# Kernel tuning notes

Measured on AMD Instinct MI355X. Metric: run time of the kernel, lower is better.

The kernel has to match this reference:

```python
import jax, jax.numpy as jnp
import numpy as np

DELTA = 2.0

def _pearson(x, y):
    vx = x - jnp.mean(x)
    vy = y - jnp.mean(y)
    return jnp.sum(vx * vy) / (jnp.sqrt(jnp.sum(vx ** 2)) * jnp.sqrt(jnp.sum(vy ** 2)))

def setup_inputs() -> dict:
    key = jax.random.key(0)
    k1, k2 = jax.random.split(key)
    n = 4000000
    output = jax.random.normal(k1, (n, 6), dtype=jnp.float32)
    label = jax.random.normal(k2, (n, 1), dtype=jnp.float32)
    return {"output": output, "label": label}

def reference(output, label):
    # output: [n, 6] = [q0, q1, q2, q3, q4, q]; label: [n, 1]
    target = label[:, 0]  # [n]

    # Pearson correlation of each of the 6 prediction columns vs label
    plcc = [_pearson(output[:, i], target) for i in range(6)]

    # Per-sample weighted pseudo-Huber loss (vectorized over batch)
    diff = output - label                      # [n, 6] (pred - target)
    huber = DELTA ** 2 * (jnp.sqrt(1.0 + (diff / DELTA) ** 2) - 1.0)  # [n, 6]
    alpha_head = 0.2 * jnp.tanh(diff[:, :5]) ** 2                     # [n, 5]
    alpha = jnp.concatenate([alpha_head, jnp.ones_like(diff[:, 5:6])], axis=1)  # [n, 6]
    loss_old = jnp.mean(jnp.sum(huber * alpha, axis=1))

    p0, p1, p2, p3, p4, p5 = plcc
    s = 5.0 - p0 - p1 - p2 - p3 - p4
    plcc_pen = ((1 - p0) ** 2 + (1 - p1) ** 2 + (1 - p2) ** 2 + (1 - p3) ** 2 + (1 - p4) ** 2) / s
    loss = loss_old + plcc_pen + (1.0 - p5)
    return loss
```

## Files before the change

### kernel.cpp

```cpp
#include <hip/hip_runtime.h>
#include <math.h>

static constexpr int BLOCK     = 256;
static constexpr int NACC      = 21;
static constexpr int PSTRIDE   = 24;
static constexpr int TILE_ROWS = 1024;
static constexpr int TILE_F4   = TILE_ROWS * 6 / 4;
static constexpr int MAXBLOCKS = 2048;

__device__ __forceinline__ void async_f4(const float4* g, float4* l) {
    __builtin_amdgcn_global_load_lds(
        (const __attribute__((address_space(1))) void*)g,
        (__attribute__((address_space(3))) void*)l,
        16, 0, 0);
}

__device__ __forceinline__ float fast_tanh_sq(float d) {
    float e = __expf(2.0f * d);
    float r = __builtin_amdgcn_rcpf(e + 1.0f);
    float t = 1.0f - 2.0f * r;
    return t * t;
}

__device__ __forceinline__ void row_accum(float acc[NACC], const float x[6], float y) {
    acc[18] += y;
    acc[19] += y * y;
    float rowh = 0.0f;
#pragma unroll
    for (int c = 0; c < 6; ++c) {
        const float xv = x[c];
        acc[c]      += xv;
        acc[6 + c]  += xv * xv;
        acc[12 + c] += xv * y;
        const float d   = xv - y;
        const float hub = 4.0f * (__builtin_amdgcn_sqrtf(1.0f + 0.25f * d * d) - 1.0f);
        const float al  = (c < 5) ? (0.2f * fast_tanh_sq(d)) : 1.0f;
        rowh += hub * al;
    }
    acc[20] += rowh;
}

__device__ __forceinline__ void chunk_accum(float acc[NACC],
                                            const float4 a, const float4 b,
                                            const float4 c, const float2 y2) {
    const float r0v[6] = {a.x, a.y, a.z, a.w, b.x, b.y};
    const float r1v[6] = {b.z, b.w, c.x, c.y, c.z, c.w};
    row_accum(acc, r0v, y2.x);
    row_accum(acc, r1v, y2.y);
}

__global__ __launch_bounds__(BLOCK) void huber_partial_kernel(
    const float* __restrict__ out6,
    const float* __restrict__ lab,
    float* __restrict__ part,
    int n)
{
    __shared__ float4 tile[TILE_F4];
    __shared__ float  red[BLOCK / 64][NACC];

    float acc[NACC];
#pragma unroll
    for (int k = 0; k < NACC; ++k) acc[k] = 0.0f;

    const int t  = threadIdx.x;
    const int n2 = n & ~1;
    const int full_tiles = n2 / TILE_ROWS;
    const int tail_start = full_tiles * TILE_ROWS;

    const float4* gsrc = reinterpret_cast<const float4*>(out6);
    const float2* lab2 = reinterpret_cast<const float2*>(lab);

    for (int tl = blockIdx.x; tl < full_tiles; tl += gridDim.x) {
        const long long basef4 = (long long)tl * TILE_F4;

#pragma unroll
        for (int k = 0; k < 6; ++k)
            async_f4(&gsrc[basef4 + k * BLOCK + t], &tile[k * BLOCK + t]);

        const float2 yA = lab2[(size_t)tl * (TILE_ROWS / 2) + t];
        const float2 yB = lab2[(size_t)tl * (TILE_ROWS / 2) + BLOCK + t];

        __syncthreads();

        chunk_accum(acc, tile[3 * t + 0], tile[3 * t + 1], tile[3 * t + 2], yA);
        chunk_accum(acc, tile[TILE_F4 / 2 + 3 * t + 0],
                         tile[TILE_F4 / 2 + 3 * t + 1],
                         tile[TILE_F4 / 2 + 3 * t + 2], yB);

        __syncthreads();
    }

    if (blockIdx.x == 0) {
        for (int r = tail_start + 2 * t; r + 1 < n2 + 1; r += 2 * BLOCK) {
            if (r + 1 >= n2) break;
            const long long g = (long long)r * 3 / 2;
            chunk_accum(acc, gsrc[g], gsrc[g + 1], gsrc[g + 2], lab2[r >> 1]);
        }
        if ((n & 1) && t == 0) {
            const size_t row = (size_t)n - 1;
            float xr[6];
#pragma unroll
            for (int c = 0; c < 6; ++c) xr[c] = out6[row * 6 + c];
            row_accum(acc, xr, lab[row]);
        }
    }

#pragma unroll
    for (int k = 0; k < NACC; ++k) {
        float v = acc[k];
#pragma unroll
        for (int off = 32; off > 0; off >>= 1)
            v += __shfl_down(v, off, 64);
        acc[k] = v;
    }

    const int wave = t >> 6;
    const int lane = t & 63;
    if (lane == 0) {
#pragma unroll
        for (int k = 0; k < NACC; ++k) red[wave][k] = acc[k];
    }
    __syncthreads();
    if (t < NACC) {
        float s = 0.0f;
#pragma unroll
        for (int w = 0; w < BLOCK / 64; ++w) s += red[w][t];
        part[(size_t)blockIdx.x * PSTRIDE + t] = s;
    }
}

__global__ __launch_bounds__(BLOCK) void huber_final_kernel(
    const float* __restrict__ part, int nblocks, int n, float* __restrict__ out)
{
    __shared__ double sred[BLOCK / 64][NACC];

    double acc[NACC];
#pragma unroll
    for (int k = 0; k < NACC; ++k) acc[k] = 0.0;

    for (int b = threadIdx.x; b < nblocks; b += BLOCK) {
        const float* p = part + (size_t)b * PSTRIDE;
        const float4* p4 = reinterpret_cast<const float4*>(p);
#pragma unroll
        for (int q = 0; q < 5; ++q) {
            const float4 v = p4[q];
            acc[q * 4 + 0] += (double)v.x;
            acc[q * 4 + 1] += (double)v.y;
            acc[q * 4 + 2] += (double)v.z;
            acc[q * 4 + 3] += (double)v.w;
        }
        acc[20] += (double)p[20];
    }

#pragma unroll
    for (int k = 0; k < NACC; ++k) {
        double v = acc[k];
#pragma unroll
        for (int off = 32; off > 0; off >>= 1)
            v += __shfl_down(v, off, 64);
        acc[k] = v;
    }

    const int wave = threadIdx.x >> 6;
    const int lane = threadIdx.x & 63;
    if (lane == 0) {
#pragma unroll
        for (int k = 0; k < NACC; ++k) sred[wave][k] = acc[k];
    }
    __syncthreads();

    if (threadIdx.x == 0) {
        double tot[NACC];
#pragma unroll
        for (int k = 0; k < NACC; ++k) {
            double s = 0.0;
#pragma unroll
            for (int w = 0; w < BLOCK / 64; ++w) s += sred[w][k];
            tot[k] = s;
        }

        const double dn  = (double)n;
        const double Sy  = tot[18];
        const double Syy = tot[19];
        const double vary = Syy - Sy * Sy / dn;
        double pc[6];
#pragma unroll
        for (int c = 0; c < 6; ++c) {
            const double Sx  = tot[c];
            const double Sxx = tot[6 + c];
            const double Sxy = tot[12 + c];
            const double cov  = Sxy - Sx * Sy / dn;
            const double varx = Sxx - Sx * Sx / dn;
            pc[c] = cov / (sqrt(varx) * sqrt(vary));
        }
        const double loss_old = tot[20] / dn;
        const double s = 5.0 - pc[0] - pc[1] - pc[2] - pc[3] - pc[4];
        double pen = 0.0;
#pragma unroll
        for (int c = 0; c < 5; ++c) pen += (1.0 - pc[c]) * (1.0 - pc[c]);
        pen /= s;
        const double loss = loss_old + pen + (1.0 - pc[5]);
        out[0] = (float)loss;
    }
}

extern "C" void kernel_launch(void* const* d_in, const int* in_sizes, int n_in,
                              void* d_out, int out_size, void* d_ws, size_t ws_size,
                              hipStream_t stream) {
    const float* out6 = (const float*)d_in[0];
    const float* lab  = (const float*)d_in[1];
    float* out = (float*)d_out;
    const int n = in_sizes[1];

    const int n2 = n & ~1;
    int full_tiles = n2 / TILE_ROWS;
    if (full_tiles < 1) full_tiles = 1;

    int nblocks = MAXBLOCKS;
    const int maxb = (int)(ws_size / (PSTRIDE * sizeof(float)));
    if (nblocks > maxb)       nblocks = maxb;
    if (nblocks > full_tiles) nblocks = full_tiles;
    if (nblocks < 1)          nblocks = 1;

    float* part = (float*)d_ws;
    hipLaunchKernelGGL(huber_partial_kernel, dim3(nblocks), dim3(BLOCK), 0, stream,
                       out6, lab, part, n);
    hipLaunchKernelGGL(huber_final_kernel, dim3(1), dim3(BLOCK), 0, stream,
                       part, nblocks, n, out);
}
```

Baseline: 163.0 us.

## Double-buffer per-wave async LDS loads to overlap memory with compute

Replaces the block-wide tile loop, which used two __syncthreads per tile, with independent per-wave 128-row tiles that are double-buffered in LDS. The next tile's data and labels are fetched with async global_load_lds while the current tile is processed, and waves are ordered with s_waitcnt vmcnt instead of barriers. Labels now also go through LDS using 4-byte async loads. This aims to hide memory latency and remove block-level syncs, but it depends on the hand-written vmcnt counts being correct and makes the label loads much smaller.

```diff
diff --git a/kernel.cpp b/kernel.cpp
--- a/kernel.cpp
+++ b/kernel.cpp
@@ -1,18 +1,25 @@
 #include <hip/hip_runtime.h>
 #include <math.h>
 
-static constexpr int BLOCK     = 256;
-static constexpr int NACC      = 21;
-static constexpr int PSTRIDE   = 24;
-static constexpr int TILE_ROWS = 1024;
-static constexpr int TILE_F4   = TILE_ROWS * 6 / 4;
-static constexpr int MAXBLOCKS = 2048;
+static constexpr int BLOCK      = 256;
+static constexpr int WAVES      = BLOCK / 64;
+static constexpr int NACC       = 21;
+static constexpr int PSTRIDE    = 24;
+static constexpr int WTILE_ROWS = 128;
+static constexpr int WTILE_F4   = WTILE_ROWS * 6 / 4;
+static constexpr int MAXBLOCKS  = 2048;
 
 __device__ __forceinline__ void async_f4(const float4* g, float4* l) {
     __builtin_amdgcn_global_load_lds(
         (const __attribute__((address_space(1))) void*)g,
         (__attribute__((address_space(3))) void*)l,
         16, 0, 0);
+}
+__device__ __forceinline__ void async_f1(const float* g, float* l) {
+    __builtin_amdgcn_global_load_lds(
+        (const __attribute__((address_space(1))) void*)g,
+        (__attribute__((address_space(3))) void*)l,
+        4, 0, 0);
 }
 
 __device__ __forceinline__ float fast_tanh_sq(float d) {
@@ -55,53 +62,60 @@
     float* __restrict__ part,
     int n)
 {
-    __shared__ float4 tile[TILE_F4];
-    __shared__ float  red[BLOCK / 64][NACC];
+    __shared__ __align__(16) float4 sdat[WAVES][2][WTILE_F4];
+    __shared__ __align__(16) float  slab[WAVES][2][WTILE_ROWS];
+    __shared__ float red[WAVES][NACC];
 
     float acc[NACC];
 #pragma unroll
     for (int k = 0; k < NACC; ++k) acc[k] = 0.0f;
 
-    const int t  = threadIdx.x;
-    const int n2 = n & ~1;
-    const int full_tiles = n2 / TILE_ROWS;
-    const int tail_start = full_tiles * TILE_ROWS;
-
+    const int t = threadIdx.x;
+    const int w = t >> 6;
+    const int l = t & 63;
+
+    const long long tiles = (long long)n / WTILE_ROWS;
+    const int nws = gridDim.x * WAVES;
     const float4* gsrc = reinterpret_cast<const float4*>(out6);
-    const float2* lab2 = reinterpret_cast<const float2*>(lab);
-
-    for (int tl = blockIdx.x; tl < full_tiles; tl += gridDim.x) {
-        const long long basef4 = (long long)tl * TILE_F4;
-
-#pragma unroll
-        for (int k = 0; k < 6; ++k)
-            async_f4(&gsrc[basef4 + k * BLOCK + t], &tile[k * BLOCK + t]);
-
-        const float2 yA = lab2[(size_t)tl * (TILE_ROWS / 2) + t];
-        const float2 yB = lab2[(size_t)tl * (TILE_ROWS / 2) + BLOCK + t];
-
-        __syncthreads();
-
-        chunk_accum(acc, tile[3 * t + 0], tile[3 * t + 1], tile[3 * t + 2], yA);
-        chunk_accum(acc, tile[TILE_F4 / 2 + 3 * t + 0],
-                         tile[TILE_F4 / 2 + 3 * t + 1],
-                         tile[TILE_F4 / 2 + 3 * t + 2], yB);
-
-        __syncthreads();
-    }
-
-    if (blockIdx.x == 0) {
-        for (int r = tail_start + 2 * t; r + 1 < n2 + 1; r += 2 * BLOCK) {
-            if (r + 1 >= n2) break;
-            const long long g = (long long)r * 3 / 2;
-            chunk_accum(acc, gsrc[g], gsrc[g + 1], gsrc[g + 2], lab2[r >> 1]);
-        }
-        if ((n & 1) && t == 0) {
-            const size_t row = (size_t)n - 1;
+
+    auto issue = [&](long long tile, int b) {
+        const float4* g = gsrc + tile * WTILE_F4;
+        async_f4(g + l,       &sdat[w][b][l]);
+        async_f4(g + 64 + l,  &sdat[w][b][64 + l]);
+        async_f4(g + 128 + l, &sdat[w][b][128 + l]);
+        const float* gl = lab + tile * WTILE_ROWS;
+        async_f1(gl + l,      &slab[w][b][l]);
+        async_f1(gl + 64 + l, &slab[w][b][64 + l]);
+    };
+
+    long long tc = (long long)blockIdx.x * WAVES + w;
+    int buf = 0;
+    if (tc < tiles) issue(tc, buf);
+
+    while (tc < tiles) {
+        const long long tn = tc + nws;
+        if (tn < tiles) {
+            issue(tn, buf ^ 1);
+            asm volatile("s_waitcnt vmcnt(5)" ::: "memory");
+        } else {
+            asm volatile("s_waitcnt vmcnt(0)" ::: "memory");
+        }
+        const float4 a = sdat[w][buf][3 * l + 0];
+        const float4 b = sdat[w][buf][3 * l + 1];
+        const float4 c = sdat[w][buf][3 * l + 2];
+        const float2 y2 = make_float2(slab[w][buf][2 * l],
+                                      slab[w][buf][2 * l + 1]);
+        chunk_accum(acc, a, b, c, y2);
+        buf ^= 1;
+        tc = tn;
+    }
+
+    if (blockIdx.x == 0 && w == 0) {
+        for (long long r = tiles * WTILE_ROWS + l; r < n; r += 64) {
             float xr[6];
 #pragma unroll
-            for (int c = 0; c < 6; ++c) xr[c] = out6[row * 6 + c];
-            row_accum(acc, xr, lab[row]);
+            for (int c = 0; c < 6; ++c) xr[c] = out6[r * 6 + c];
+            row_accum(acc, xr, lab[r]);
         }
     }
 
@@ -113,18 +127,15 @@
             v += __shfl_down(v, off, 64);
         acc[k] = v;
     }
-
-    const int wave = t >> 6;
-    const int lane = t & 63;
-    if (lane == 0) {
-#pragma unroll
-        for (int k = 0; k < NACC; ++k) red[wave][k] = acc[k];
+    if (l == 0) {
+#pragma unroll
+        for (int k = 0; k < NACC; ++k) red[w][k] = acc[k];
     }
     __syncthreads();
     if (t < NACC) {
         float s = 0.0f;
 #pragma unroll
-        for (int w = 0; w < BLOCK / 64; ++w) s += red[w][t];
+        for (int ww = 0; ww < WAVES; ++ww) s += red[ww][t];
         part[(size_t)blockIdx.x * PSTRIDE + t] = s;
     }
 }
@@ -212,15 +223,15 @@
     float* out = (float*)d_out;
     const int n = in_sizes[1];
 
-    const int n2 = n & ~1;
-    int full_tiles = n2 / TILE_ROWS;
-    if (full_tiles < 1) full_tiles = 1;
+    const long long tiles = (long long)n / WTILE_ROWS;
+    long long want = (tiles + WAVES - 1) / WAVES;
+    if (want < 1) want = 1;
 
     int nblocks = MAXBLOCKS;
     const int maxb = (int)(ws_size / (PSTRIDE * sizeof(float)));
-    if (nblocks > maxb)       nblocks = maxb;
-    if (nblocks > full_tiles) nblocks = full_tiles;
-    if (nblocks < 1)          nblocks = 1;
+    if (nblocks > maxb) nblocks = maxb;
+    if ((long long)nblocks > want) nblocks = (int)want;
+    if (nblocks < 1) nblocks = 1;
 
     float* part = (float*)d_ws;
     hipLaunchKernelGGL(huber_partial_kernel, dim3(nblocks), dim3(BLOCK), 0, stream,
```

New measurement: 164.0 us. No clear change (+0.6%).
